# Performance work log

Measured on AMD Instinct MI355X. Metric: run time of the kernel, lower is better.

## Reference

```python
import jax, jax.numpy as jnp
import numpy as np

N = 131072   # total nodes (B*C)
D = 128      # hidden_dim
H = 4        # gat_heads == hgt_heads
HD = 32      # head dim
T = 3        # number of edge types
E = 262144   # edges per edge type
B = 512      # graphs
EPS = 1e-6
SLOPE = 0.2  # LeakyReLU negative slope (module-wide and GAT internal)


def _rmsnorm(x, scale):
    return scale * x * jax.lax.rsqrt(jnp.mean(x * x, axis=-1, keepdims=True) + EPS)


def _gat(x, ei, W, a_src, a_dst, b):
    """HeteroConv(sum) of per-edge-type GATConv (concat heads, self-loops)."""
    loops = jnp.arange(N)

    def one(ei_t, W_t, as_t, ad_t):
        h = (x @ W_t).reshape(N, H, HD)                         # [N,H,HD]
        src = jnp.concatenate([ei_t[0], loops])                 # add self loops
        dst = jnp.concatenate([ei_t[1], loops])
        a = jax.nn.leaky_relu((h * as_t).sum(-1)[src] + (h * ad_t).sum(-1)[dst], SLOPE)  # [E',H]
        m = jax.ops.segment_max(a, dst, num_segments=N)
        ex = jnp.exp(a - m[dst])
        s = jax.ops.segment_sum(ex, dst, num_segments=N)
        alpha = ex / s[dst]                                     # segment softmax per dst
        out = jax.ops.segment_sum(h[src] * alpha[..., None], dst, num_segments=N)
        return out.reshape(N, D)

    return jax.vmap(one)(ei, W, a_src, a_dst).sum(0) + b.sum(0)


def _hgt(x, ei, kw, kb, qw, qb, vw, vb, rel_k, rel_v, rel_p, aw, ab, skip):
    """HGTConv, single node type, T edge types; softmax over all incoming edges."""
    k = (x @ kw + kb).reshape(N, H, HD)
    q = (x @ qw + qb).reshape(N, H, HD)
    v = (x @ vw + vb).reshape(N, H, HD)
    kt = jnp.einsum('nhd,thde->tnhe', k, rel_k)                 # relation-specific keys
    vt = jnp.einsum('nhd,thde->tnhe', v, rel_v)
    k_msg = jax.vmap(lambda a, i: a[i])(kt, ei[:, 0]).reshape(T * E, H, HD)
    v_msg = jax.vmap(lambda a, i: a[i])(vt, ei[:, 0]).reshape(T * E, H, HD)
    dst = ei[:, 1].reshape(T * E)
    p = jnp.broadcast_to(rel_p[:, None, :], (T, E, H)).reshape(T * E, H)
    score = (q[dst] * k_msg).sum(-1) * p / np.sqrt(HD)          # [T*E,H]
    m = jax.ops.segment_max(score, dst, num_segments=N)
    ex = jnp.exp(score - m[dst])
    s = jax.ops.segment_sum(ex, dst, num_segments=N)
    alpha = ex / s[dst]
    out = jax.ops.segment_sum(alpha[..., None] * v_msg, dst, num_segments=N).reshape(N, D)
    out = jax.nn.gelu(out, approximate=False) @ aw + ab
    g = jax.nn.sigmoid(skip)
    return g * out + (1.0 - g) * x


def _res(x_old, x_new, scale):
    # norm -> (dropout is identity in eval) -> residual -> LeakyReLU(0.2)
    return jax.nn.leaky_relu(x_old + _rmsnorm(x_new, scale), SLOPE)


def setup_inputs() -> dict:
    key = jax.random.key(0)
    ks = iter(jax.random.split(key, 48))

    def nrm(shape, std=0.1):
        return jax.random.normal(next(ks), shape, jnp.float32) * std

    inp = {}
    inp['x_cell'] = nrm((N, D), 1.0)
    inp['x_cell_embedded'] = nrm((N, D), 1.0)
    inp['z_h'] = nrm((B, D), 1.0)
    inp['edge_index'] = jax.random.randint(next(ks), (T, 2, E), 0, N)
    for l in ('gat1', 'gat2'):
        inp[l + '_w'] = nrm((T, D, H * HD))
        inp[l + '_att_src'] = nrm((T, H, HD))
        inp[l + '_att_dst'] = nrm((T, H, HD))
        inp[l + '_b'] = jnp.zeros((T, D), jnp.float32)
    inp['norm1_s'] = jnp.ones((D,), jnp.float32)
    inp['norm2_s'] = jnp.ones((D,), jnp.float32)
    inp['norm3_s'] = jnp.ones((D,), jnp.float32)
    for nm in ('k', 'q', 'v'):
        inp['hgt_%s_w' % nm] = nrm((D, D))
        inp['hgt_%s_b' % nm] = jnp.zeros((D,), jnp.float32)
    inp['hgt_rel_k'] = nrm((T, H, HD, HD))
    inp['hgt_rel_v'] = nrm((T, H, HD, HD))
    inp['hgt_rel_p'] = jnp.ones((T, H), jnp.float32)
    inp['hgt_a_w'] = nrm((D, D))
    inp['hgt_a_b'] = jnp.zeros((D,), jnp.float32)
    inp['hgt_skip'] = jnp.ones((), jnp.float32)
    inp['inj_w'] = nrm((D, D))
    inp['inj_b'] = jnp.zeros((D,), jnp.float32)
    inp['film_w1'] = nrm((D, 2 * D))
    inp['film_b1'] = jnp.zeros((2 * D,), jnp.float32)
    inp['film_w2'] = nrm((2 * D, 2 * D), 0.001)
    inp['film_b2'] = jnp.zeros((2 * D,), jnp.float32)
    inp['batch_size'] = B
    return inp


def reference(x_cell, x_cell_embedded, z_h, edge_index,
              gat1_w, gat1_att_src, gat1_att_dst, gat1_b,
              gat2_w, gat2_att_src, gat2_att_dst, gat2_b,
              norm1_s, norm2_s, norm3_s,
              hgt_k_w, hgt_k_b, hgt_q_w, hgt_q_b, hgt_v_w, hgt_v_b,
              hgt_rel_k, hgt_rel_v, hgt_rel_p, hgt_a_w, hgt_a_b, hgt_skip,
              inj_w, inj_b, film_w1, film_b1, film_w2, film_b2, batch_size):
    x1 = _res(x_cell, _gat(x_cell, edge_index, gat1_w, gat1_att_src, gat1_att_dst, gat1_b), norm1_s)
    x2 = _res(x1, _gat(x1, edge_index, gat2_w, gat2_att_src, gat2_att_dst, gat2_b), norm2_s)
    x3 = _res(x2, _hgt(x2, edge_index, hgt_k_w, hgt_k_b, hgt_q_w, hgt_q_b, hgt_v_w, hgt_v_b,
                       hgt_rel_k, hgt_rel_v, hgt_rel_p, hgt_a_w, hgt_a_b, hgt_skip), norm3_s)
    x3 = x3 + x_cell_embedded @ inj_w + inj_b                   # input injection
    # FiLM (per-graph z, fixed batch mode)
    gb = jax.nn.gelu(z_h @ film_w1 + film_b1, approximate=False) @ film_w2 + film_b2
    gamma, beta = jnp.split(gb, 2, axis=-1)
    gamma = 0.1 * jnp.tanh(gamma)
    beta = 0.1 * jnp.tanh(beta)
    C = N // batch_size
    out = (1.0 + gamma)[:, None, :] * x3.reshape(batch_size, C, D) + beta[:, None, :]
    return out.reshape(N, D)
```

## Files before the change

### kernel.cpp

```cpp
#include <hip/hip_runtime.h>
#include <math.h>
#include <cstdint>

#define NN     131072
#define DDIM   128
#define NHEAD  4
#define HDIM   32
#define NTYPE  3
#define NEDGE  262144
#define NGRAPH 512
#define EPSV   1e-6f
#define SLOPEV 0.2f

typedef unsigned short bfraw;
typedef __attribute__((ext_vector_type(8))) short bf16x8;
typedef __attribute__((ext_vector_type(4))) float f32x4;

__device__ __forceinline__ float lrelu(float x){ return x >= 0.f ? x : SLOPEV*x; }
__device__ __forceinline__ float gelu_f(float x){ return 0.5f*x*(1.f+erff(x*0.70710678118654752f)); }
__device__ __forceinline__ bfraw f2bf(float f){
  unsigned int u = __float_as_uint(f);
  u += 0x7fffu + ((u >> 16) & 1u);
  return (bfraw)(u >> 16);
}
__device__ __forceinline__ float4 ld_bf4(const bfraw* p){
  uint2 u = *reinterpret_cast<const uint2*>(p);
  float4 r;
  r.x = __uint_as_float(u.x << 16); r.y = __uint_as_float(u.x & 0xffff0000u);
  r.z = __uint_as_float(u.y << 16); r.w = __uint_as_float(u.y & 0xffff0000u);
  return r;
}
__device__ __forceinline__ bf16x8 pack_bf8(const float* p){
  float4 u = *reinterpret_cast<const float4*>(p);
  float4 v = *reinterpret_cast<const float4*>(p+4);
  bf16x8 r;
  r[0]=(short)f2bf(u.x); r[1]=(short)f2bf(u.y); r[2]=(short)f2bf(u.z); r[3]=(short)f2bf(u.w);
  r[4]=(short)f2bf(v.x); r[5]=(short)f2bf(v.y); r[6]=(short)f2bf(v.z); r[7]=(short)f2bf(v.w);
  return r;
}

__global__ void fill_k(float* __restrict__ p, float v, int n){
  int i = blockIdx.x*blockDim.x + threadIdx.x;
  int stride = gridDim.x*blockDim.x;
  for (; i < n; i += stride) p[i] = v;
}

__global__ void hist_k(const int* __restrict__ ei, int* __restrict__ deg){
  int idx = blockIdx.x*256 + threadIdx.x;
  int t = idx >> 18, e = idx & (NEDGE-1);
  int d = ei[(long)t*2*NEDGE + NEDGE + e];
  atomicAdd(&deg[t*NN + d], 1);
}

__global__ void scan_a_k(const int* __restrict__ deg, int* __restrict__ rp,
                         int* __restrict__ csum){
  __shared__ int sh[256];
  int t = blockIdx.y, chunk = blockIdx.x, tid = threadIdx.x;
  const int* dp = deg + (long)t*NN + chunk*2048 + tid*8;
  int v[8]; int s = 0;
  #pragma unroll
  for (int i=0;i<8;i++){ v[i] = dp[i]; s += v[i]; }
  sh[tid] = s; __syncthreads();
  for (int off=1; off<256; off<<=1){
    int x = (tid>=off) ? sh[tid-off] : 0;
    __syncthreads();
    sh[tid] += x;
    __syncthreads();
  }
  int run = sh[tid] - s;
  int* op = rp + (long)t*(NN+1) + chunk*2048 + tid*8;
  #pragma unroll
  for (int i=0;i<8;i++){ op[i] = run; run += v[i]; }
  if (tid == 255) csum[t*64 + chunk] = sh[255];
}

__global__ void scan_b_k(int* __restrict__ csum){
  __shared__ int sh[64];
  int t = blockIdx.x, tid = threadIdx.x;
  int s = csum[t*64 + tid];
  sh[tid] = s; __syncthreads();
  for (int off=1; off<64; off<<=1){
    int x = (tid>=off) ? sh[tid-off] : 0;
    __syncthreads();
    sh[tid] += x;
    __syncthreads();
  }
  csum[t*64 + tid] = sh[tid] - s;
}

__global__ void scan_c_k(int* __restrict__ rp, const int* __restrict__ csum){
  int t = blockIdx.y, chunk = blockIdx.x, tid = threadIdx.x;
  int add = csum[t*64 + chunk];
  int* op = rp + (long)t*(NN+1) + chunk*2048 + tid*8;
  #pragma unroll
  for (int i=0;i<8;i++) op[i] += add;
  if (chunk == 63 && tid == 255) rp[(long)t*(NN+1) + NN] = NEDGE;
}

__global__ void scatter_k(const int* __restrict__ ei, const int* __restrict__ rp,
                          int* __restrict__ cnt, int* __restrict__ srcs){
  int idx = blockIdx.x*256 + threadIdx.x;
  int t = idx >> 18, e = idx & (NEDGE-1);
  int s = ei[(long)t*2*NEDGE + e];
  int d = ei[(long)t*2*NEDGE + NEDGE + e];
  int pos = rp[(long)t*(NN+1) + d] + atomicAdd(&cnt[t*NN + d], 1);
  srcs[(long)t*NEDGE + pos] = s;
}

__global__ void wswz_k(const float* g0a, const float* g0b, const float* g0c,
                       const float* g1a, const float* g1b, const float* g1c,
                       const float* qw,
                       const float* wk, const float* wv,
                       const float* aw, const float* injw,
                       bfraw* __restrict__ Wall)
{
  int y = blockIdx.y;
  const float* src;
  switch(y){
    case 0: src = g0a; break;  case 1: src = g0b; break;  case 2: src = g0c; break;
    case 3: src = g1a; break;  case 4: src = g1b; break;  case 5: src = g1c; break;
    case 6: src = qw; break;
    case 7: case 8: case 9: src = wk + (long)(y-7)*16384; break;
    case 10: case 11: case 12: src = wv + (long)(y-10)*16384; break;
    case 13: src = aw; break;
    default: src = injw; break;
  }
  int i = blockIdx.x*256 + threadIdx.x;
  int j = i & 7, lane = (i>>3) & 63, kc = (i>>9) & 3, nt = i >> 11;
  int k = kc*32 + ((lane>>4)<<3) + j;
  int n = nt*16 + (lane & 15);
  Wall[(long)y*16384 + i] = f2bf(src[k*DDIM + n]);
}

__global__ void gatproj_k(const float* __restrict__ w, const float* __restrict__ asrc,
                          const float* __restrict__ adst, bfraw* __restrict__ out)
{
  int i = blockIdx.x*256 + threadIdx.x;
  int j = i & 7, lane = (i>>3) & 63, kc = (i>>9) & 3, nt = i >> 11;
  int k = kc*32 + ((lane>>4)<<3) + j;
  int n = nt*16 + (lane & 15);
  float s = 0.f;
  if (n < 24){
    int t = n >> 3, sd = (n >> 2) & 1, hh = n & 3;
    const float* a  = (sd ? adst : asrc) + ((long)t*NHEAD + hh)*HDIM;
    const float* wr = w + ((long)t*DDIM + k)*DDIM + hh*HDIM;
    #pragma unroll 8
    for (int dd=0; dd<HDIM; dd++) s += wr[dd]*a[dd];
  }
  out[i] = f2bf(s);
}

__device__ __forceinline__ void load_afrags_bf16(const bfraw* __restrict__ A,
    long blockRow, int tid, bf16x8 a0[4], bf16x8 a1[4])
{
  const int w = tid >> 6, lane = tid & 63;
  const long rowA = blockRow + w*32 + (lane & 15);
  const bfraw* A0 = A + rowA*DDIM + ((lane>>4)<<3);
  #pragma unroll
  for (int kc=0;kc<4;kc++){
    a0[kc] = *reinterpret_cast<const bf16x8*>(A0 + kc*32);
    a1[kc] = *reinterpret_cast<const bf16x8*>(A0 + 16*DDIM + kc*32);
  }
}

__device__ __forceinline__ void load_afrags_f32(const float* __restrict__ A,
    long blockRow, int tid, bf16x8 a0[4], bf16x8 a1[4])
{
  const int w = tid >> 6, lane = tid & 63;
  const long rowA = blockRow + w*32 + (lane & 15);
  const float* A0 = A + rowA*DDIM + ((lane>>4)<<3);
  #pragma unroll
  for (int kc=0;kc<4;kc++){
    a0[kc] = pack_bf8(A0 + kc*32);
    a1[kc] = pack_bf8(A0 + 16*DDIM + kc*32);
  }
}

__device__ __forceinline__ void mfma_128(const bfraw* Wl, int lane,
    bf16x8 a0[4], bf16x8 a1[4], f32x4 acc0[8], f32x4 acc1[8])
{
  const f32x4 zz = {0.f,0.f,0.f,0.f};
  #pragma unroll
  for (int nt=0;nt<8;nt++){ acc0[nt]=zz; acc1[nt]=zz; }
  #pragma unroll
  for (int nt=0;nt<8;nt++){
    #pragma unroll
    for (int kc=0;kc<4;kc++){
      bf16x8 b = *reinterpret_cast<const bf16x8*>(Wl + ((nt*4+kc)*64 + lane)*8);
      acc0[nt] = __builtin_amdgcn_mfma_f32_16x16x32_bf16(a0[kc], b, acc0[nt], 0, 0, 0);
      acc1[nt] = __builtin_amdgcn_mfma_f32_16x16x32_bf16(a1[kc], b, acc1[nt], 0, 0, 0);
    }
  }
}

__device__ __forceinline__ void gemm_store_bf16(f32x4 acc0[8], f32x4 acc1[8],
    const float* bias, bfraw* __restrict__ Cb, long blockRow, int tid)
{
  const int w = tid>>6, lane = tid&63, q = lane>>4;
  #pragma unroll
  for (int g=0; g<2; g++){
    #pragma unroll
    for (int nt=0;nt<8;nt++){
      int col = nt*16 + (lane & 15);
      float bv = bias ? bias[col] : 0.f;
      #pragma unroll
      for (int r=0;r<4;r++){
        long row = blockRow + w*32 + g*16 + q*4 + r;
        float v = (g ? acc1[nt][r] : acc0[nt][r]) + bv;
        Cb[row*DDIM + col] = f2bf(v);
      }
    }
  }
}

__global__ __launch_bounds__(256) void gemm_out_k(
    const bfraw* __restrict__ A, const bfraw* __restrict__ Wsw,
    const float* __restrict__ bias, bfraw* __restrict__ Cb)
{
  __shared__ bfraw Wl[16384];
  const int tid = threadIdx.x;
  const long blockRow = (long)blockIdx.x * 128;
  #pragma unroll
  for (int i=0;i<8;i++)
    *reinterpret_cast<uint4*>(Wl + (i*256+tid)*8) =
        *reinterpret_cast<const uint4*>(Wsw + (i*256+tid)*8);
  __syncthreads();
  bf16x8 a0[4], a1[4];
  load_afrags_bf16(A, blockRow, tid, a0, a1);
  f32x4 acc0[8], acc1[8];
  mfma_128(Wl, tid & 63, a0, a1, acc0, acc1);
  gemm_store_bf16(acc0, acc1, bias, Cb, blockRow, tid);
}

__global__ __launch_bounds__(256) void gemm3_k(
    const bfraw* __restrict__ Ab, const float* __restrict__ Af,
    const bfraw* __restrict__ W0, const bfraw* __restrict__ W1,
    const bfraw* __restrict__ W2,
    const float* __restrict__ b0, const float* __restrict__ b1,
    const float* __restrict__ b2,
    bfraw* __restrict__ O0, bfraw* __restrict__ O1, bfraw* __restrict__ O2,
    const bfraw* __restrict__ Psw, float* __restrict__ SS)
{
  __shared__ bfraw Wl[16384];
  const int tid = threadIdx.x;
  const long blockRow = (long)blockIdx.x * 128;
  const int w = tid >> 6, lane = tid & 63;
  bf16x8 a0[4], a1[4];
  if (Af) load_afrags_f32(Af, blockRow, tid, a0, a1);
  else    load_afrags_bf16(Ab, blockRow, tid, a0, a1);
  const bfraw* Ws[3] = {W0, W1, W2};
  const float* bs[3] = {b0, b1, b2};
  bfraw* Os[3] = {O0, O1, O2};
  #pragma unroll
  for (int t=0;t<3;t++){
    __syncthreads();
    #pragma unroll
    for (int i=0;i<8;i++)
      *reinterpret_cast<uint4*>(Wl + (i*256+tid)*8) =
          *reinterpret_cast<const uint4*>(Ws[t] + (i*256+tid)*8);
    __syncthreads();
    f32x4 acc0[8], acc1[8];
    mfma_128(Wl, lane, a0, a1, acc0, acc1);
    gemm_store_bf16(acc0, acc1, bs[t], Os[t], blockRow, tid);
  }
  if (Psw){
    __syncthreads();
    #pragma unroll
    for (int i=0;i<2;i++)
      *reinterpret_cast<uint4*>(Wl + (i*256+tid)*8) =
          *reinterpret_cast<const uint4*>(Psw + (i*256+tid)*8);
    __syncthreads();
    const f32x4 zz = {0.f,0.f,0.f,0.f};
    f32x4 acc0[2], acc1[2];
    #pragma unroll
    for (int nt=0;nt<2;nt++){ acc0[nt]=zz; acc1[nt]=zz; }
    #pragma unroll
    for (int nt=0;nt<2;nt++){
      #pragma unroll
      for (int kc=0;kc<4;kc++){
        bf16x8 b = *reinterpret_cast<const bf16x8*>(Wl + ((nt*4+kc)*64 + lane)*8);
        acc0[nt] = __builtin_amdgcn_mfma_f32_16x16x32_bf16(a0[kc], b, acc0[nt], 0, 0, 0);
        acc1[nt] = __builtin_amdgcn_mfma_f32_16x16x32_bf16(a1[kc], b, acc1[nt], 0, 0, 0);
      }
    }
    const int q = lane >> 4;
    #pragma unroll
    for (int g=0; g<2; g++){
      #pragma unroll
      for (int nt=0;nt<2;nt++){
        int col = nt*16 + (lane & 15);
        if (col < 24){
          int tt = col >> 3, c = col & 7;
          #pragma unroll
          for (int r=0;r<4;r++){
            long row = blockRow + w*32 + g*16 + q*4 + r;
            SS[(((long)tt*NN + row)<<3) + c] = (g ? acc1[nt][r] : acc0[nt][r]);
          }
        }
      }
    }
  }
}

__global__ __launch_bounds__(256) void gemm_r3film_k(
    const bfraw* __restrict__ Aattn, const bfraw* __restrict__ Waw,
    const float* __restrict__ ab, const float* __restrict__ X,
    const float* __restrict__ norm, const float* __restrict__ skip,
    const float* __restrict__ xemb, const bfraw* __restrict__ Winj,
    const float* __restrict__ injb, const float* __restrict__ gbt,
    float* __restrict__ out)
{
  __shared__ bfraw Wl[16384];
  const int tid = threadIdx.x;
  const long blockRow = (long)blockIdx.x * 128;
  #pragma unroll
  for (int i=0;i<8;i++)
    *reinterpret_cast<uint4*>(Wl + (i*256+tid)*8) =
        *reinterpret_cast<const uint4*>(Waw + (i*256+tid)*8);
  __syncthreads();
  bf16x8 a0[4], a1[4];
  load_afrags_bf16(Aattn, blockRow, tid, a0, a1);
  f32x4 accA0[8], accA1[8];
  mfma_128(Wl, tid & 63, a0, a1, accA0, accA1);
  __syncthreads();
  #pragma unroll
  for (int i=0;i<8;i++)
    *reinterpret_cast<uint4*>(Wl + (i*256+tid)*8) =
        *reinterpret_cast<const uint4*>(Winj + (i*256+tid)*8);
  __syncthreads();
  load_afrags_f32(xemb, blockRow, tid, a0, a1);
  f32x4 accB0[8], accB1[8];
  mfma_128(Wl, tid & 63, a0, a1, accB0, accB1);
  const int w = tid>>6, lane = tid&63, q = lane>>4;
  const float gsk = 1.f/(1.f + __expf(-skip[0]));
  #pragma unroll
  for (int g=0; g<2; g++){
    #pragma unroll
    for (int r=0;r<4;r++){
      long row = blockRow + w*32 + g*16 + q*4 + r;
      float vv[8], xx[8];
      float sq = 0.f;
      #pragma unroll
      for (int nt=0;nt<8;nt++){
        int col = nt*16 + (lane & 15);
        float oA = (g ? accA1[nt][r] : accA0[nt][r]) + ab[col];
        float xo = X[row*DDIM + col];
        float v  = gsk*oA + (1.f-gsk)*xo;
        vv[nt] = v; xx[nt] = xo; sq += v*v;
      }
      sq += __shfl_xor(sq, 1, 64);
      sq += __shfl_xor(sq, 2, 64);
      sq += __shfl_xor(sq, 4, 64);
      sq += __shfl_xor(sq, 8, 64);
      float rr = rsqrtf(sq*(1.f/DDIM) + EPSV);
      long gi = row >> 8;
      #pragma unroll
      for (int nt=0;nt<8;nt++){
        int col = nt*16 + (lane & 15);
        float x3 = lrelu(xx[nt] + norm[col]*vv[nt]*rr);
        float vB = (g ? accB1[nt][r] : accB0[nt][r]) + injb[col] + x3;
        out[row*DDIM + col] = (1.f + gbt[gi*256 + col])*vB + gbt[gi*256 + 128 + col];
      }
    }
  }
}

__global__ __launch_bounds__(256) void gat_fused_k(
    const int* __restrict__ rp, const int* __restrict__ srcs,
    const bfraw* __restrict__ H0, const bfraw* __restrict__ H1,
    const bfraw* __restrict__ H2, const float* __restrict__ SS,
    const float* __restrict__ gatb, const float* __restrict__ xold,
    const float* __restrict__ norm, float* __restrict__ X, bfraw* __restrict__ Xb)
{
  int node = blockIdx.x*8 + (threadIdx.x >> 5);
  int l = threadIdx.x & 31;
  int hd = l >> 3;
  const bfraw* Hs[3] = {H0, H1, H2};
  float dsv[3], ssl[3]; float4 hsl[3]; int beg[3], end[3];
  #pragma unroll
  for (int t=0; t<3; t++){
    const float* St = SS + ((long)t*NN)*8;
    dsv[t] = St[(long)node*8 + 4 + hd];
    ssl[t] = St[(long)node*8 + hd];
    hsl[t] = ld_bf4(Hs[t] + (long)node*DDIM + l*4);
    beg[t] = rp[t*(NN+1) + node];
    end[t] = rp[t*(NN+1) + node + 1];
  }
  float tx=0.f, ty=0.f, tz=0.f, tw=0.f;
  #pragma unroll
  for (int t=0; t<3; t++){
    const bfraw* Ht = Hs[t];
    const float* St = SS + ((long)t*NN)*8;
    const int* sp = srcs + (long)t*NEDGE;
    const float d = dsv[t];
    float e = __expf(lrelu(ssl[t] + d));
    float lA = e, lB = 0.f;
    float4 aA = make_float4(e*hsl[t].x, e*hsl[t].y, e*hsl[t].z, e*hsl[t].w);
    float4 aB = make_float4(0.f,0.f,0.f,0.f);
    int p = beg[t];
    for (; p+1 < end[t]; p += 2){
      int s0 = sp[p], s1 = sp[p+1];
      float v0 = St[(long)s0*8 + hd];
      float v1 = St[(long)s1*8 + hd];
      float4 h0 = ld_bf4(Ht + (long)s0*DDIM + l*4);
      float4 h1 = ld_bf4(Ht + (long)s1*DDIM + l*4);
      float e0 = __expf(lrelu(v0 + d));
      float e1 = __expf(lrelu(v1 + d));
      lA += e0; lB += e1;
      aA.x += e0*h0.x; aA.y += e0*h0.y; aA.z += e0*h0.z; aA.w += e0*h0.w;
      aB.x += e1*h1.x; aB.y += e1*h1.y; aB.z += e1*h1.z; aB.w += e1*h1.w;
    }
    if (p < end[t]){
      int s0 = sp[p];
      float e0 = __expf(lrelu(St[(long)s0*8 + hd] + d));
      float4 h0 = ld_bf4(Ht + (long)s0*DDIM + l*4);
      lA += e0;
      aA.x += e0*h0.x; aA.y += e0*h0.y; aA.z += e0*h0.z; aA.w += e0*h0.w;
    }
    float inv = 1.f/(lA + lB);
    tx += (aA.x+aB.x)*inv; ty += (aA.y+aB.y)*inv;
    tz += (aA.z+aB.z)*inv; tw += (aA.w+aB.w)*inv;
  }
  int f = l*4;
  tx += gatb[f]   + gatb[DDIM+f]   + gatb[2*DDIM+f];
  ty += gatb[f+1] + gatb[DDIM+f+1] + gatb[2*DDIM+f+1];
  tz += gatb[f+2] + gatb[DDIM+f+2] + gatb[2*DDIM+f+2];
  tw += gatb[f+3] + gatb[DDIM+f+3] + gatb[2*DDIM+f+3];
  float sq = tx*tx + ty*ty + tz*tz + tw*tw;
  sq += __shfl_xor(sq, 1, 64);
  sq += __shfl_xor(sq, 2, 64);
  sq += __shfl_xor(sq, 4, 64);
  sq += __shfl_xor(sq, 8, 64);
  sq += __shfl_xor(sq, 16, 64);
  float r = rsqrtf(sq*(1.f/DDIM) + EPSV);
  float4 x4 = *reinterpret_cast<const float4*>(xold + (long)node*DDIM + f);
  float4 o;
  o.x = lrelu(x4.x + norm[f]  *tx*r);
  o.y = lrelu(x4.y + norm[f+1]*ty*r);
  o.z = lrelu(x4.z + norm[f+2]*tz*r);
  o.w = lrelu(x4.w + norm[f+3]*tw*r);
  *reinterpret_cast<float4*>(X + (long)node*DDIM + f) = o;
  unsigned int lo = ((unsigned int)f2bf(o.y) << 16) | f2bf(o.x);
  unsigned int hi = ((unsigned int)f2bf(o.w) << 16) | f2bf(o.z);
  *reinterpret_cast<uint2*>(Xb + (long)node*DDIM + f) = make_uint2(lo, hi);
}

__global__ void fold_k(const float* __restrict__ w, const float* __restrict__ b,
                       const float* __restrict__ rel, const float* __restrict__ scl,
                       float* __restrict__ Weff, float* __restrict__ beff)
{
  int idx = blockIdx.x*256 + threadIdx.x;
  if (idx >= NTYPE*DDIM*DDIM) return;
  int he = idx & 127, c = (idx >> 7) & 127, t = idx >> 14;
  int h = he >> 5, e = he & 31;
  float fs = scl ? scl[t*NHEAD + h]*0.17677669529663687f : 1.f;
  const float* wrow = w + (long)c*DDIM + h*HDIM;
  const float* relm = rel + ((long)(t*NHEAD + h)*HDIM)*HDIM + e;
  float s = 0.f;
  #pragma unroll 8
  for (int d=0; d<HDIM; d++) s += wrow[d] * relm[d*HDIM];
  Weff[(long)t*DDIM*DDIM + (long)c*DDIM + he] = s*fs;
  if (c == 0){
    float sb = 0.f;
    #pragma unroll 8
    for (int d=0; d<HDIM; d++) sb += b[h*HDIM+d] * relm[d*HDIM];
    beff[(long)t*DDIM + he] = sb*fs;
  }
}

__global__ __launch_bounds__(256) void hgt_score2_k(
    const int* __restrict__ rp, const int* __restrict__ srcs,
    const bfraw* __restrict__ qb, const bfraw* __restrict__ kt0,
    const bfraw* __restrict__ kt1, float* __restrict__ E)
{
  int node = blockIdx.x*8 + (threadIdx.x >> 5);
  int l = threadIdx.x & 31;
  int hd = l >> 3, sub = l & 7;
  float4 qv = ld_bf4(qb + (long)node*DDIM + l*4);
  #pragma unroll
  for (int t=0; t<2; t++){
    const bfraw* kt = t ? kt1 : kt0;
    const int* sp = srcs + (long)t*NEDGE;
    float* Et = E + (long)t*NEDGE*4;
    int beg = rp[t*(NN+1) + node], end = rp[t*(NN+1) + node + 1];
    int p = beg;
    for (; p+1 < end; p += 2){
      int s0 = sp[p], s1 = sp[p+1];
      float4 k0 = ld_bf4(kt + (long)s0*DDIM + l*4);
      float4 k1 = ld_bf4(kt + (long)s1*DDIM + l*4);
      float d0 = qv.x*k0.x + qv.y*k0.y + qv.z*k0.z + qv.w*k0.w;
      float d1 = qv.x*k1.x + qv.y*k1.y + qv.z*k1.z + qv.w*k1.w;
      d0 += __shfl_xor(d0, 1, 64);  d1 += __shfl_xor(d1, 1, 64);
      d0 += __shfl_xor(d0, 2, 64);  d1 += __shfl_xor(d1, 2, 64);
      d0 += __shfl_xor(d0, 4, 64);  d1 += __shfl_xor(d1, 4, 64);
      if (sub == 0){
        Et[(long)p*4 + hd]     = __expf(d0);
        Et[(long)(p+1)*4 + hd] = __expf(d1);
      }
    }
    if (p < end){
      int s0 = sp[p];
      float4 k0 = ld_bf4(kt + (long)s0*DDIM + l*4);
      float d0 = qv.x*k0.x + qv.y*k0.y + qv.z*k0.z + qv.w*k0.w;
      d0 += __shfl_xor(d0, 1, 64);
      d0 += __shfl_xor(d0, 2, 64);
      d0 += __shfl_xor(d0, 4, 64);
      if (sub == 0) Et[(long)p*4 + hd] = __expf(d0);
    }
  }
}

__global__ __launch_bounds__(256) void hgt_score1_k(
    const int* __restrict__ rp, const int* __restrict__ srcs,
    const bfraw* __restrict__ qb, const bfraw* __restrict__ kt,
    float* __restrict__ E)
{
  int node = blockIdx.x*8 + (threadIdx.x >> 5);
  int l = threadIdx.x & 31;
  int hd = l >> 3, sub = l & 7;
  float4 qv = ld_bf4(qb + (long)node*DDIM + l*4);
  int beg = rp[node], end = rp[node+1];
  int p = beg;
  for (; p+1 < end; p += 2){
    int s0 = srcs[p], s1 = srcs[p+1];
    float4 k0 = ld_bf4(kt + (long)s0*DDIM + l*4);
    float4 k1 = ld_bf4(kt + (long)s1*DDIM + l*4);
    float d0 = qv.x*k0.x + qv.y*k0.y + qv.z*k0.z + qv.w*k0.w;
    float d1 = qv.x*k1.x + qv.y*k1.y + qv.z*k1.z + qv.w*k1.w;
    d0 += __shfl_xor(d0, 1, 64);  d1 += __shfl_xor(d1, 1, 64);
    d0 += __shfl_xor(d0, 2, 64);  d1 += __shfl_xor(d1, 2, 64);
    d0 += __shfl_xor(d0, 4, 64);  d1 += __shfl_xor(d1, 4, 64);
    if (sub == 0){
      E[(long)p*4 + hd]     = __expf(d0);
      E[(long)(p+1)*4 + hd] = __expf(d1);
    }
  }
  if (p < end){
    int s0 = srcs[p];
    float4 k0 = ld_bf4(kt + (long)s0*DDIM + l*4);
    float d0 = qv.x*k0.x + qv.y*k0.y + qv.z*k0.z + qv.w*k0.w;
    d0 += __shfl_xor(d0, 1, 64);
    d0 += __shfl_xor(d0, 2, 64);
    d0 += __shfl_xor(d0, 4, 64);
    if (sub == 0) E[(long)p*4 + hd] = __expf(d0);
  }
}

__global__ __launch_bounds__(256) void hgt_acc_fused_k(
    const int* __restrict__ rp, const int* __restrict__ srcs,
    const float* __restrict__ E, const bfraw* __restrict__ V0,
    const bfraw* __restrict__ V1, const bfraw* __restrict__ V2,
    bfraw* __restrict__ out)
{
  int node = blockIdx.x*8 + (threadIdx.x >> 5);
  int l = threadIdx.x & 31;
  int hd = l >> 3;
  float axA=0.f, ayA=0.f, azA=0.f, awA=0.f, lsA=0.f;
  float axB=0.f, ayB=0.f, azB=0.f, awB=0.f, lsB=0.f;
  const bfraw* Vs[3] = {V0, V1, V2};
  #pragma unroll
  for (int t=0; t<3; t++){
    const bfraw* Vt = Vs[t];
    const float* Ep = E + (long)t*NEDGE*4;
    const int* sp = srcs + (long)t*NEDGE;
    int beg = rp[t*(NN+1) + node], end = rp[t*(NN+1) + node + 1];
    int p = beg;
    for (; p+1 < end; p += 2){
      int s0 = sp[p], s1 = sp[p+1];
      float e0 = Ep[(long)p*4 + hd];
      float e1 = Ep[(long)(p+1)*4 + hd];
      float4 v0 = ld_bf4(Vt + (long)s0*DDIM + l*4);
      float4 v1 = ld_bf4(Vt + (long)s1*DDIM + l*4);
      axA += e0*v0.x; ayA += e0*v0.y; azA += e0*v0.z; awA += e0*v0.w; lsA += e0;
      axB += e1*v1.x; ayB += e1*v1.y; azB += e1*v1.z; awB += e1*v1.w; lsB += e1;
    }
    if (p < end){
      int s0 = sp[p];
      float e0 = Ep[(long)p*4 + hd];
      float4 v0 = ld_bf4(Vt + (long)s0*DDIM + l*4);
      axA += e0*v0.x; ayA += e0*v0.y; azA += e0*v0.z; awA += e0*v0.w; lsA += e0;
    }
  }
  float lsum = lsA + lsB;
  float inv = (lsum > 0.f) ? 1.f/lsum : 0.f;
  float o0 = gelu_f((axA+axB)*inv), o1 = gelu_f((ayA+ayB)*inv);
  float o2 = gelu_f((azA+azB)*inv), o3 = gelu_f((awA+awB)*inv);
  unsigned int lo = ((unsigned int)f2bf(o1) << 16) | f2bf(o0);
  unsigned int hi = ((unsigned int)f2bf(o3) << 16) | f2bf(o2);
  *reinterpret_cast<uint2*>(out + (long)node*DDIM + l*4) = make_uint2(lo, hi);
}

__global__ void film1_k(const float* __restrict__ z, const float* __restrict__ w1,
                        const float* __restrict__ b1, float* __restrict__ f1)
{
  int idx = blockIdx.x*256 + threadIdx.x;
  if (idx >= NGRAPH*256) return;
  int j = idx & 255, b = idx >> 8;
  const float* zr = z + (long)b*DDIM;
  float s = b1[j];
  for (int k=0;k<DDIM;k++) s += zr[k] * w1[(long)k*256 + j];
  f1[idx] = gelu_f(s);
}

__global__ void film2_k(const float* __restrict__ f1, const float* __restrict__ w2,
                        const float* __restrict__ b2, float* __restrict__ gb)
{
  int idx = blockIdx.x*256 + threadIdx.x;
  if (idx >= NGRAPH*256) return;
  int j = idx & 255, b = idx >> 8;
  const float* fr = f1 + (long)b*256;
  float s = b2[j];
  for (int k=0;k<256;k++) s += fr[k] * w2[(long)k*256 + j];
  gb[idx] = 0.1f*tanhf(s);
}

extern "C" void kernel_launch(void* const* d_in, const int* in_sizes, int n_in,
                              void* d_out, int out_size, void* d_ws, size_t ws_size,
                              hipStream_t stream)
{
  (void)in_sizes; (void)n_in; (void)out_size; (void)ws_size;
  const float* x_cell = (const float*)d_in[0];
  const float* x_emb  = (const float*)d_in[1];
  const float* z_h    = (const float*)d_in[2];
  const int*   ei     = (const int*)d_in[3];
  const float* gw[2]  = {(const float*)d_in[4],  (const float*)d_in[8]};
  const float* gas[2] = {(const float*)d_in[5],  (const float*)d_in[9]};
  const float* gad[2] = {(const float*)d_in[6],  (const float*)d_in[10]};
  const float* gbi[2] = {(const float*)d_in[7],  (const float*)d_in[11]};
  const float* norm1  = (const float*)d_in[12];
  const float* norm2  = (const float*)d_in[13];
  const float* norm3  = (const float*)d_in[14];
  const float* kw = (const float*)d_in[15]; const float* kb = (const float*)d_in[16];
  const float* qw = (const float*)d_in[17]; const float* qb = (const float*)d_in[18];
  const float* vw = (const float*)d_in[19]; const float* vb = (const float*)d_in[20];
  const float* relk = (const float*)d_in[21];
  const float* relv = (const float*)d_in[22];
  const float* relp = (const float*)d_in[23];
  const float* aw = (const float*)d_in[24]; const float* ab = (const float*)d_in[25];
  const float* skip = (const float*)d_in[26];
  const float* injw = (const float*)d_in[27]; const float* injb = (const float*)d_in[28];
  const float* fw1 = (const float*)d_in[29]; const float* fb1 = (const float*)d_in[30];
  const float* fw2 = (const float*)d_in[31]; const float* fb2 = (const float*)d_in[32];

  const long ND = (long)NN*DDIM;
  float* X    = (float*)d_ws;
  float* K    = X + ND;
  bfraw* Xb   = (bfraw*)(K + ND);
  bfraw* Hb   = Xb + ND;
  float* Sbuf = (float*)(Hb + ND);
  float* sA   = Sbuf + (long)NTYPE*NEDGE*4;
  float* sB   = sA + (long)NN*4;
  float* WkE  = sB + (long)NN*4;
  float* bkE  = WkE + (long)NTYPE*DDIM*DDIM;
  float* WvE  = bkE + (long)NTYPE*DDIM;
  float* bvE  = WvE + (long)NTYPE*DDIM*DDIM;
  bfraw* Pswz = (bfraw*)(bvE + (long)NTYPE*DDIM);
  bfraw* Wall = Pswz + (long)2*4096;
  float* f1b  = (float*)(Wall + (long)15*16384);
  float* gbb  = f1b + (long)NGRAPH*256;
  int*   deg  = (int*)(gbb + (long)NGRAPH*256);
  int*   rp   = deg + (long)NTYPE*NN;
  int*   srcs = rp  + (long)NTYPE*(NN+1);
  int*   csum = srcs + (long)NTYPE*NEDGE;

  bfraw* Kb0 = (bfraw*)K;
  bfraw* Kb1 = Kb0 + ND;

  const dim3 b256(256);
  float* NF = nullptr;
  bfraw* NB = nullptr; (void)NB; (void)sA; (void)sB;

  fill_k<<<256, b256, 0, stream>>>((float*)deg, 0.f, NTYPE*NN);
  hist_k<<<(NTYPE*NEDGE)/256, b256, 0, stream>>>(ei, deg);
  scan_a_k<<<dim3(64, NTYPE), b256, 0, stream>>>(deg, rp, csum);
  scan_b_k<<<NTYPE, 64, 0, stream>>>(csum);
  scan_c_k<<<dim3(64, NTYPE), b256, 0, stream>>>(rp, csum);
  fill_k<<<256, b256, 0, stream>>>((float*)deg, 0.f, NTYPE*NN);
  scatter_k<<<(NTYPE*NEDGE)/256, b256, 0, stream>>>(ei, rp, deg, srcs);

  fold_k<<<(NTYPE*DDIM*DDIM)/256, b256, 0, stream>>>(kw, kb, relk, relp, WkE, bkE);
  fold_k<<<(NTYPE*DDIM*DDIM)/256, b256, 0, stream>>>(vw, vb, relv, NF, WvE, bvE);
  wswz_k<<<dim3(64, 15), b256, 0, stream>>>(
      gw[0], gw[0]+16384, gw[0]+32768,
      gw[1], gw[1]+16384, gw[1]+32768,
      qw, WkE, WvE, aw, injw, Wall);
  gatproj_k<<<16, b256, 0, stream>>>(gw[0], gas[0], gad[0], Pswz);
  gatproj_k<<<16, b256, 0, stream>>>(gw[1], gas[1], gad[1], Pswz + 4096);

  film1_k<<<(NGRAPH*256)/256, b256, 0, stream>>>(z_h, fw1, fb1, f1b);
  film2_k<<<(NGRAPH*256)/256, b256, 0, stream>>>(f1b, fw2, fb2, gbb);

  for (int layer=0; layer<2; layer++){
    gemm3_k<<<NN/128, b256, 0, stream>>>(
        Xb, (layer==0) ? x_cell : NF,
        Wall + (long)(layer*3+0)*16384, Wall + (long)(layer*3+1)*16384,
        Wall + (long)(layer*3+2)*16384,
        NF, NF, NF,
        Hb, Kb0, Kb1,
        Pswz + (long)layer*4096, Sbuf);
    gat_fused_k<<<NN/8, b256, 0, stream>>>(
        rp, srcs, Hb, Kb0, Kb1, Sbuf, gbi[layer],
        (layer==0) ? x_cell : X, (layer==0) ? norm1 : norm2, X, Xb);
  }

  gemm3_k<<<NN/128, b256, 0, stream>>>(
      Xb, NF, Wall + (long)6*16384, Wall + (long)7*16384, Wall + (long)8*16384,
      qb, bkE, bkE + DDIM,
      Kb0, Hb, Kb1, nullptr, nullptr);
  hgt_score2_k<<<NN/8, b256, 0, stream>>>(rp, srcs, Kb0, Hb, Kb1, Sbuf);
  gemm_out_k<<<NN/128, b256, 0, stream>>>(Xb, Wall + (long)9*16384, bkE + 2*DDIM, Hb);
  hgt_score1_k<<<NN/8, b256, 0, stream>>>(rp + 2*(NN+1), srcs + 2*NEDGE, Kb0, Hb,
      Sbuf + (long)2*NEDGE*4);
  gemm3_k<<<NN/128, b256, 0, stream>>>(
      Xb, NF, Wall + (long)10*16384, Wall + (long)11*16384, Wall + (long)12*16384,
      bvE, bvE + DDIM, bvE + 2*DDIM,
      Hb, Kb0, Kb1, nullptr, nullptr);
  hgt_acc_fused_k<<<NN/8, b256, 0, stream>>>(rp, srcs, Sbuf, Hb, Kb0, Kb1, Xb);
  gemm_r3film_k<<<NN/128, b256, 0, stream>>>(
      Xb, Wall + (long)13*16384, ab, X, norm3, skip,
      x_emb, Wall + (long)14*16384, injb, gbb, (float*)d_out);
}
```

Before: 878.1 us.

## Interleave per-type edge loops and fuse HGT Q/K projections into one GEMM

The GAT aggregation, HGT score and HGT accumulate kernels now walk all three edge types in one predicated loop, two edges per type per iteration, instead of running the types one after another. The aim is to keep up to six independent gathers in flight per iteration to hide memory latency. gemm3_k gains an optional fourth weight matrix, so Q and all three relation keys come from a single launch, and the separate score2, gemm_out and score1 kernels are replaced by one hgt_score3_k. Q is written to the output buffer as scratch space. The cost is extra register pressure and wasted masked loads when degrees differ between types.

```diff
diff --git a/kernel.cpp b/kernel.cpp
--- a/kernel.cpp
+++ b/kernel.cpp
@@ -213,25 +213,6 @@
   }
 }
 
-__global__ __launch_bounds__(256) void gemm_out_k(
-    const bfraw* __restrict__ A, const bfraw* __restrict__ Wsw,
-    const float* __restrict__ bias, bfraw* __restrict__ Cb)
-{
-  __shared__ bfraw Wl[16384];
-  const int tid = threadIdx.x;
-  const long blockRow = (long)blockIdx.x * 128;
-  #pragma unroll
-  for (int i=0;i<8;i++)
-    *reinterpret_cast<uint4*>(Wl + (i*256+tid)*8) =
-        *reinterpret_cast<const uint4*>(Wsw + (i*256+tid)*8);
-  __syncthreads();
-  bf16x8 a0[4], a1[4];
-  load_afrags_bf16(A, blockRow, tid, a0, a1);
-  f32x4 acc0[8], acc1[8];
-  mfma_128(Wl, tid & 63, a0, a1, acc0, acc1);
-  gemm_store_bf16(acc0, acc1, bias, Cb, blockRow, tid);
-}
-
 __global__ __launch_bounds__(256) void gemm3_k(
     const bfraw* __restrict__ Ab, const float* __restrict__ Af,
     const bfraw* __restrict__ W0, const bfraw* __restrict__ W1,
@@ -239,7 +220,9 @@
     const float* __restrict__ b0, const float* __restrict__ b1,
     const float* __restrict__ b2,
     bfraw* __restrict__ O0, bfraw* __restrict__ O1, bfraw* __restrict__ O2,
-    const bfraw* __restrict__ Psw, float* __restrict__ SS)
+    const bfraw* __restrict__ Psw, float* __restrict__ SS,
+    const bfraw* __restrict__ W3, const float* __restrict__ b3,
+    bfraw* __restrict__ O3)
 {
   __shared__ bfraw Wl[16384];
   const int tid = threadIdx.x;
@@ -262,6 +245,17 @@
     f32x4 acc0[8], acc1[8];
     mfma_128(Wl, lane, a0, a1, acc0, acc1);
     gemm_store_bf16(acc0, acc1, bs[t], Os[t], blockRow, tid);
+  }
+  if (W3){
+    __syncthreads();
+    #pragma unroll
+    for (int i=0;i<8;i++)
+      *reinterpret_cast<uint4*>(Wl + (i*256+tid)*8) =
+          *reinterpret_cast<const uint4*>(W3 + (i*256+tid)*8);
+    __syncthreads();
+    f32x4 acc0[8], acc1[8];
+    mfma_128(Wl, lane, a0, a1, acc0, acc1);
+    gemm_store_bf16(acc0, acc1, b3, O3, blockRow, tid);
   }
   if (Psw){
     __syncthreads();
@@ -375,52 +369,72 @@
   int node = blockIdx.x*8 + (threadIdx.x >> 5);
   int l = threadIdx.x & 31;
   int hd = l >> 3;
-  const bfraw* Hs[3] = {H0, H1, H2};
-  float dsv[3], ssl[3]; float4 hsl[3]; int beg[3], end[3];
-  #pragma unroll
-  for (int t=0; t<3; t++){
-    const float* St = SS + ((long)t*NN)*8;
-    dsv[t] = St[(long)node*8 + 4 + hd];
-    ssl[t] = St[(long)node*8 + hd];
-    hsl[t] = ld_bf4(Hs[t] + (long)node*DDIM + l*4);
-    beg[t] = rp[t*(NN+1) + node];
-    end[t] = rp[t*(NN+1) + node + 1];
-  }
-  float tx=0.f, ty=0.f, tz=0.f, tw=0.f;
-  #pragma unroll
-  for (int t=0; t<3; t++){
-    const bfraw* Ht = Hs[t];
-    const float* St = SS + ((long)t*NN)*8;
-    const int* sp = srcs + (long)t*NEDGE;
-    const float d = dsv[t];
-    float e = __expf(lrelu(ssl[t] + d));
-    float lA = e, lB = 0.f;
-    float4 aA = make_float4(e*hsl[t].x, e*hsl[t].y, e*hsl[t].z, e*hsl[t].w);
-    float4 aB = make_float4(0.f,0.f,0.f,0.f);
-    int p = beg[t];
-    for (; p+1 < end[t]; p += 2){
-      int s0 = sp[p], s1 = sp[p+1];
-      float v0 = St[(long)s0*8 + hd];
-      float v1 = St[(long)s1*8 + hd];
-      float4 h0 = ld_bf4(Ht + (long)s0*DDIM + l*4);
-      float4 h1 = ld_bf4(Ht + (long)s1*DDIM + l*4);
-      float e0 = __expf(lrelu(v0 + d));
-      float e1 = __expf(lrelu(v1 + d));
-      lA += e0; lB += e1;
-      aA.x += e0*h0.x; aA.y += e0*h0.y; aA.z += e0*h0.z; aA.w += e0*h0.w;
-      aB.x += e1*h1.x; aB.y += e1*h1.y; aB.z += e1*h1.z; aB.w += e1*h1.w;
-    }
-    if (p < end[t]){
-      int s0 = sp[p];
-      float e0 = __expf(lrelu(St[(long)s0*8 + hd] + d));
-      float4 h0 = ld_bf4(Ht + (long)s0*DDIM + l*4);
-      lA += e0;
-      aA.x += e0*h0.x; aA.y += e0*h0.y; aA.z += e0*h0.z; aA.w += e0*h0.w;
-    }
-    float inv = 1.f/(lA + lB);
-    tx += (aA.x+aB.x)*inv; ty += (aA.y+aB.y)*inv;
-    tz += (aA.z+aB.z)*inv; tw += (aA.w+aB.w)*inv;
-  }
+  const float* S0 = SS;
+  const float* S1 = SS + (long)NN*8;
+  const float* S2 = SS + (long)2*NN*8;
+  float d0 = S0[(long)node*8 + 4 + hd];
+  float d1 = S1[(long)node*8 + 4 + hd];
+  float d2 = S2[(long)node*8 + 4 + hd];
+  float z0 = S0[(long)node*8 + hd];
+  float z1 = S1[(long)node*8 + hd];
+  float z2 = S2[(long)node*8 + hd];
+  float4 h0 = ld_bf4(H0 + (long)node*DDIM + l*4);
+  float4 h1 = ld_bf4(H1 + (long)node*DDIM + l*4);
+  float4 h2 = ld_bf4(H2 + (long)node*DDIM + l*4);
+  float w0 = __expf(lrelu(z0 + d0));
+  float w1 = __expf(lrelu(z1 + d1));
+  float w2 = __expf(lrelu(z2 + d2));
+  float l0 = w0, l1 = w1, l2 = w2;
+  float4 A0 = make_float4(w0*h0.x, w0*h0.y, w0*h0.z, w0*h0.w);
+  float4 A1 = make_float4(w1*h1.x, w1*h1.y, w1*h1.z, w1*h1.w);
+  float4 A2 = make_float4(w2*h2.x, w2*h2.y, w2*h2.z, w2*h2.w);
+  int p0 = rp[node],            e0 = rp[node+1];
+  int p1 = rp[(NN+1)+node],     e1 = rp[(NN+1)+node+1];
+  int p2 = rp[2*(NN+1)+node],   e2 = rp[2*(NN+1)+node+1];
+  const int* sp0 = srcs;
+  const int* sp1 = srcs + NEDGE;
+  const int* sp2 = srcs + (long)2*NEDGE;
+  while (p0 < e0 || p1 < e1 || p2 < e2){
+    bool b0a = p0 < e0, b0b = p0+1 < e0;
+    bool b1a = p1 < e1, b1b = p1+1 < e1;
+    bool b2a = p2 < e2, b2b = p2+1 < e2;
+    int s0a = b0a ? sp0[p0]   : node;
+    int s0b = b0b ? sp0[p0+1] : node;
+    int s1a = b1a ? sp1[p1]   : node;
+    int s1b = b1b ? sp1[p1+1] : node;
+    int s2a = b2a ? sp2[p2]   : node;
+    int s2b = b2b ? sp2[p2+1] : node;
+    float v0a = S0[(long)s0a*8 + hd], v0b = S0[(long)s0b*8 + hd];
+    float v1a = S1[(long)s1a*8 + hd], v1b = S1[(long)s1b*8 + hd];
+    float v2a = S2[(long)s2a*8 + hd], v2b = S2[(long)s2b*8 + hd];
+    float4 g0a = ld_bf4(H0 + (long)s0a*DDIM + l*4);
+    float4 g0b = ld_bf4(H0 + (long)s0b*DDIM + l*4);
+    float4 g1a = ld_bf4(H1 + (long)s1a*DDIM + l*4);
+    float4 g1b = ld_bf4(H1 + (long)s1b*DDIM + l*4);
+    float4 g2a = ld_bf4(H2 + (long)s2a*DDIM + l*4);
+    float4 g2b = ld_bf4(H2 + (long)s2b*DDIM + l*4);
+    float e0a = b0a ? __expf(lrelu(v0a + d0)) : 0.f;
+    float e0b = b0b ? __expf(lrelu(v0b + d0)) : 0.f;
+    float e1a = b1a ? __expf(lrelu(v1a + d1)) : 0.f;
+    float e1b = b1b ? __expf(lrelu(v1b + d1)) : 0.f;
+    float e2a = b2a ? __expf(lrelu(v2a + d2)) : 0.f;
+    float e2b = b2b ? __expf(lrelu(v2b + d2)) : 0.f;
+    l0 += e0a + e0b; l1 += e1a + e1b; l2 += e2a + e2b;
+    A0.x += e0a*g0a.x + e0b*g0b.x; A0.y += e0a*g0a.y + e0b*g0b.y;
+    A0.z += e0a*g0a.z + e0b*g0b.z; A0.w += e0a*g0a.w + e0b*g0b.w;
+    A1.x += e1a*g1a.x + e1b*g1b.x; A1.y += e1a*g1a.y + e1b*g1b.y;
+    A1.z += e1a*g1a.z + e1b*g1b.z; A1.w += e1a*g1a.w + e1b*g1b.w;
+    A2.x += e2a*g2a.x + e2b*g2b.x; A2.y += e2a*g2a.y + e2b*g2b.y;
+    A2.z += e2a*g2a.z + e2b*g2b.z; A2.w += e2a*g2a.w + e2b*g2b.w;
+    p0 += (b0a?1:0) + (b0b?1:0);
+    p1 += (b1a?1:0) + (b1b?1:0);
+    p2 += (b2a?1:0) + (b2b?1:0);
+  }
+  float i0 = 1.f/l0, i1 = 1.f/l1, i2 = 1.f/l2;
+  float tx = A0.x*i0 + A1.x*i1 + A2.x*i2;
+  float ty = A0.y*i0 + A1.y*i1 + A2.y*i2;
+  float tz = A0.z*i0 + A1.z*i1 + A2.z*i2;
+  float tw = A0.w*i0 + A1.w*i1 + A2.w*i2;
   int f = l*4;
   tx += gatb[f]   + gatb[DDIM+f]   + gatb[2*DDIM+f];
   ty += gatb[f+1] + gatb[DDIM+f+1] + gatb[2*DDIM+f+1];
@@ -468,81 +482,67 @@
   }
 }
 
-__global__ __launch_bounds__(256) void hgt_score2_k(
+__global__ __launch_bounds__(256) void hgt_score3_k(
     const int* __restrict__ rp, const int* __restrict__ srcs,
     const bfraw* __restrict__ qb, const bfraw* __restrict__ kt0,
-    const bfraw* __restrict__ kt1, float* __restrict__ E)
+    const bfraw* __restrict__ kt1, const bfraw* __restrict__ kt2,
+    float* __restrict__ E)
 {
   int node = blockIdx.x*8 + (threadIdx.x >> 5);
   int l = threadIdx.x & 31;
   int hd = l >> 3, sub = l & 7;
   float4 qv = ld_bf4(qb + (long)node*DDIM + l*4);
-  #pragma unroll
-  for (int t=0; t<2; t++){
-    const bfraw* kt = t ? kt1 : kt0;
-    const int* sp = srcs + (long)t*NEDGE;
-    float* Et = E + (long)t*NEDGE*4;
-    int beg = rp[t*(NN+1) + node], end = rp[t*(NN+1) + node + 1];
-    int p = beg;
-    for (; p+1 < end; p += 2){
-      int s0 = sp[p], s1 = sp[p+1];
-      float4 k0 = ld_bf4(kt + (long)s0*DDIM + l*4);
-      float4 k1 = ld_bf4(kt + (long)s1*DDIM + l*4);
-      float d0 = qv.x*k0.x + qv.y*k0.y + qv.z*k0.z + qv.w*k0.w;
-      float d1 = qv.x*k1.x + qv.y*k1.y + qv.z*k1.z + qv.w*k1.w;
-      d0 += __shfl_xor(d0, 1, 64);  d1 += __shfl_xor(d1, 1, 64);
-      d0 += __shfl_xor(d0, 2, 64);  d1 += __shfl_xor(d1, 2, 64);
-      d0 += __shfl_xor(d0, 4, 64);  d1 += __shfl_xor(d1, 4, 64);
-      if (sub == 0){
-        Et[(long)p*4 + hd]     = __expf(d0);
-        Et[(long)(p+1)*4 + hd] = __expf(d1);
-      }
+  float* E0 = E;
+  float* E1 = E + (long)NEDGE*4;
+  float* E2 = E + (long)2*NEDGE*4;
+  const int* sp0 = srcs;
+  const int* sp1 = srcs + NEDGE;
+  const int* sp2 = srcs + (long)2*NEDGE;
+  int p0 = rp[node],            e0 = rp[node+1];
+  int p1 = rp[(NN+1)+node],     e1 = rp[(NN+1)+node+1];
+  int p2 = rp[2*(NN+1)+node],   e2 = rp[2*(NN+1)+node+1];
+  while (p0 < e0 || p1 < e1 || p2 < e2){
+    bool b0a = p0 < e0, b0b = p0+1 < e0;
+    bool b1a = p1 < e1, b1b = p1+1 < e1;
+    bool b2a = p2 < e2, b2b = p2+1 < e2;
+    int s0a = b0a ? sp0[p0]   : 0;
+    int s0b = b0b ? sp0[p0+1] : 0;
+    int s1a = b1a ? sp1[p1]   : 0;
+    int s1b = b1b ? sp1[p1+1] : 0;
+    int s2a = b2a ? sp2[p2]   : 0;
+    int s2b = b2b ? sp2[p2+1] : 0;
+    float4 k0a = ld_bf4(kt0 + (long)s0a*DDIM + l*4);
+    float4 k0b = ld_bf4(kt0 + (long)s0b*DDIM + l*4);
+    float4 k1a = ld_bf4(kt1 + (long)s1a*DDIM + l*4);
+    float4 k1b = ld_bf4(kt1 + (long)s1b*DDIM + l*4);
+    float4 k2a = ld_bf4(kt2 + (long)s2a*DDIM + l*4);
+    float4 k2b = ld_bf4(kt2 + (long)s2b*DDIM + l*4);
+    float d0a = qv.x*k0a.x + qv.y*k0a.y + qv.z*k0a.z + qv.w*k0a.w;
+    float d0b = qv.x*k0b.x + qv.y*k0b.y + qv.z*k0b.z + qv.w*k0b.w;
+    float d1a = qv.x*k1a.x + qv.y*k1a.y + qv.z*k1a.z + qv.w*k1a.w;
+    float d1b = qv.x*k1b.x + qv.y*k1b.y + qv.z*k1b.z + qv.w*k1b.w;
+    float d2a = qv.x*k2a.x + qv.y*k2a.y + qv.z*k2a.z + qv.w*k2a.w;
+    float d2b = qv.x*k2b.x + qv.y*k2b.y + qv.z*k2b.z + qv.w*k2b.w;
+    d0a += __shfl_xor(d0a, 1, 64); d0b += __shfl_xor(d0b, 1, 64);
+    d1a += __shfl_xor(d1a, 1, 64); d1b += __shfl_xor(d1b, 1, 64);
+    d2a += __shfl_xor(d2a, 1, 64); d2b += __shfl_xor(d2b, 1, 64);
+    d0a += __shfl_xor(d0a, 2, 64); d0b += __shfl_xor(d0b, 2, 64);
+    d1a += __shfl_xor(d1a, 2, 64); d1b += __shfl_xor(d1b, 2, 64);
+    d2a += __shfl_xor(d2a, 2, 64); d2b += __shfl_xor(d2b, 2, 64);
+    d0a += __shfl_xor(d0a, 4, 64); d0b += __shfl_xor(d0b, 4, 64);
+    d1a += __shfl_xor(d1a, 4, 64); d1b += __shfl_xor(d1b, 4, 64);
+    d2a += __shfl_xor(d2a, 4, 64); d2b += __shfl_xor(d2b, 4, 64);
+    if (sub == 0){
+      if (b0a) E0[(long)p0*4 + hd]     = __expf(d0a);
+      if (b0b) E0[(long)(p0+1)*4 + hd] = __expf(d0b);
+      if (b1a) E1[(long)p1*4 + hd]     = __expf(d1a);
+      if (b1b) E1[(long)(p1+1)*4 + hd] = __expf(d1b);
+      if (b2a) E2[(long)p2*4 + hd]     = __expf(d2a);
+      if (b2b) E2[(long)(p2+1)*4 + hd] = __expf(d2b);
     }
-    if (p < end){
-      int s0 = sp[p];
-      float4 k0 = ld_bf4(kt + (long)s0*DDIM + l*4);
-      float d0 = qv.x*k0.x + qv.y*k0.y + qv.z*k0.z + qv.w*k0.w;
-      d0 += __shfl_xor(d0, 1, 64);
-      d0 += __shfl_xor(d0, 2, 64);
-      d0 += __shfl_xor(d0, 4, 64);
-      if (sub == 0) Et[(long)p*4 + hd] = __expf(d0);
-    }
-  }
-}
-
-__global__ __launch_bounds__(256) void hgt_score1_k(
-    const int* __restrict__ rp, const int* __restrict__ srcs,
-    const bfraw* __restrict__ qb, const bfraw* __restrict__ kt,
-    float* __restrict__ E)
-{
-  int node = blockIdx.x*8 + (threadIdx.x >> 5);
-  int l = threadIdx.x & 31;
-  int hd = l >> 3, sub = l & 7;
-  float4 qv = ld_bf4(qb + (long)node*DDIM + l*4);
-  int beg = rp[node], end = rp[node+1];
-  int p = beg;
-  for (; p+1 < end; p += 2){
-    int s0 = srcs[p], s1 = srcs[p+1];
-    float4 k0 = ld_bf4(kt + (long)s0*DDIM + l*4);
-    float4 k1 = ld_bf4(kt + (long)s1*DDIM + l*4);
-    float d0 = qv.x*k0.x + qv.y*k0.y + qv.z*k0.z + qv.w*k0.w;
-    float d1 = qv.x*k1.x + qv.y*k1.y + qv.z*k1.z + qv.w*k1.w;
-    d0 += __shfl_xor(d0, 1, 64);  d1 += __shfl_xor(d1, 1, 64);
-    d0 += __shfl_xor(d0, 2, 64);  d1 += __shfl_xor(d1, 2, 64);
-    d0 += __shfl_xor(d0, 4, 64);  d1 += __shfl_xor(d1, 4, 64);
-    if (sub == 0){
-      E[(long)p*4 + hd]     = __expf(d0);
-      E[(long)(p+1)*4 + hd] = __expf(d1);
-    }
-  }
-  if (p < end){
-    int s0 = srcs[p];
-    float4 k0 = ld_bf4(kt + (long)s0*DDIM + l*4);
-    float d0 = qv.x*k0.x + qv.y*k0.y + qv.z*k0.z + qv.w*k0.w;
-    d0 += __shfl_xor(d0, 1, 64);
-    d0 += __shfl_xor(d0, 2, 64);
-    d0 += __shfl_xor(d0, 4, 64);
-    if (sub == 0) E[(long)p*4 + hd] = __expf(d0);
+    p0 += (b0a?1:0) + (b0b?1:0);
+    p1 += (b1a?1:0) + (b1b?1:0);
+    p2 += (b2a?1:0) + (b2b?1:0);
   }
 }
 
@@ -555,36 +555,59 @@
   int node = blockIdx.x*8 + (threadIdx.x >> 5);
   int l = threadIdx.x & 31;
   int hd = l >> 3;
-  float axA=0.f, ayA=0.f, azA=0.f, awA=0.f, lsA=0.f;
-  float axB=0.f, ayB=0.f, azB=0.f, awB=0.f, lsB=0.f;
-  const bfraw* Vs[3] = {V0, V1, V2};
-  #pragma unroll
-  for (int t=0; t<3; t++){
-    const bfraw* Vt = Vs[t];
-    const float* Ep = E + (long)t*NEDGE*4;
-    const int* sp = srcs + (long)t*NEDGE;
-    int beg = rp[t*(NN+1) + node], end = rp[t*(NN+1) + node + 1];
-    int p = beg;
-    for (; p+1 < end; p += 2){
-      int s0 = sp[p], s1 = sp[p+1];
-      float e0 = Ep[(long)p*4 + hd];
-      float e1 = Ep[(long)(p+1)*4 + hd];
-      float4 v0 = ld_bf4(Vt + (long)s0*DDIM + l*4);
-      float4 v1 = ld_bf4(Vt + (long)s1*DDIM + l*4);
-      axA += e0*v0.x; ayA += e0*v0.y; azA += e0*v0.z; awA += e0*v0.w; lsA += e0;
-      axB += e1*v1.x; ayB += e1*v1.y; azB += e1*v1.z; awB += e1*v1.w; lsB += e1;
-    }
-    if (p < end){
-      int s0 = sp[p];
-      float e0 = Ep[(long)p*4 + hd];
-      float4 v0 = ld_bf4(Vt + (long)s0*DDIM + l*4);
-      axA += e0*v0.x; ayA += e0*v0.y; azA += e0*v0.z; awA += e0*v0.w; lsA += e0;
-    }
-  }
-  float lsum = lsA + lsB;
+  const float* E0 = E;
+  const float* E1 = E + (long)NEDGE*4;
+  const float* E2 = E + (long)2*NEDGE*4;
+  const int* sp0 = srcs;
+  const int* sp1 = srcs + NEDGE;
+  const int* sp2 = srcs + (long)2*NEDGE;
+  int p0 = rp[node],            e0 = rp[node+1];
+  int p1 = rp[(NN+1)+node],     e1 = rp[(NN+1)+node+1];
+  int p2 = rp[2*(NN+1)+node],   e2 = rp[2*(NN+1)+node+1];
+  float4 A0 = make_float4(0.f,0.f,0.f,0.f);
+  float4 A1 = make_float4(0.f,0.f,0.f,0.f);
+  float4 A2 = make_float4(0.f,0.f,0.f,0.f);
+  float l0 = 0.f, l1 = 0.f, l2 = 0.f;
+  while (p0 < e0 || p1 < e1 || p2 < e2){
+    bool b0a = p0 < e0, b0b = p0+1 < e0;
+    bool b1a = p1 < e1, b1b = p1+1 < e1;
+    bool b2a = p2 < e2, b2b = p2+1 < e2;
+    int s0a = b0a ? sp0[p0]   : 0;
+    int s0b = b0b ? sp0[p0+1] : 0;
+    int s1a = b1a ? sp1[p1]   : 0;
+    int s1b = b1b ? sp1[p1+1] : 0;
+    int s2a = b2a ? sp2[p2]   : 0;
+    int s2b = b2b ? sp2[p2+1] : 0;
+    long q0a = b0a ? (long)p0 : 0, q0b = b0b ? (long)(p0+1) : 0;
+    long q1a = b1a ? (long)p1 : 0, q1b = b1b ? (long)(p1+1) : 0;
+    long q2a = b2a ? (long)p2 : 0, q2b = b2b ? (long)(p2+1) : 0;
+    float w0a = E0[q0a*4 + hd], w0b = E0[q0b*4 + hd];
+    float w1a = E1[q1a*4 + hd], w1b = E1[q1b*4 + hd];
+    float w2a = E2[q2a*4 + hd], w2b = E2[q2b*4 + hd];
+    float4 g0a = ld_bf4(V0 + (long)s0a*DDIM + l*4);
+    float4 g0b = ld_bf4(V0 + (long)s0b*DDIM + l*4);
+    float4 g1a = ld_bf4(V1 + (long)s1a*DDIM + l*4);
+    float4 g1b = ld_bf4(V1 + (long)s1b*DDIM + l*4);
+    float4 g2a = ld_bf4(V2 + (long)s2a*DDIM + l*4);
+    float4 g2b = ld_bf4(V2 + (long)s2b*DDIM + l*4);
+    w0a = b0a ? w0a : 0.f; w0b = b0b ? w0b : 0.f;
+    w1a = b1a ? w1a : 0.f; w1b = b1b ? w1b : 0.f;
+    w2a = b2a ? w2a : 0.f; w2b = b2b ? w2b : 0.f;
+    l0 += w0a + w0b; l1 += w1a + w1b; l2 += w2a + w2b;
+    A0.x += w0a*g0a.x + w0b*g0b.x; A0.y += w0a*g0a.y + w0b*g0b.y;
+    A0.z += w0a*g0a.z + w0b*g0b.z; A0.w += w0a*g0a.w + w0b*g0b.w;
+    A1.x += w1a*g1a.x + w1b*g1b.x; A1.y += w1a*g1a.y + w1b*g1b.y;
+    A1.z += w1a*g1a.z + w1b*g1b.z; A1.w += w1a*g1a.w + w1b*g1b.w;
+    A2.x += w2a*g2a.x + w2b*g2b.x; A2.y += w2a*g2a.y + w2b*g2b.y;
+    A2.z += w2a*g2a.z + w2b*g2b.z; A2.w += w2a*g2a.w + w2b*g2b.w;
+    p0 += (b0a?1:0) + (b0b?1:0);
+    p1 += (b1a?1:0) + (b1b?1:0);
+    p2 += (b2a?1:0) + (b2b?1:0);
+  }
+  float lsum = l0 + l1 + l2;
   float inv = (lsum > 0.f) ? 1.f/lsum : 0.f;
-  float o0 = gelu_f((axA+axB)*inv), o1 = gelu_f((ayA+ayB)*inv);
-  float o2 = gelu_f((azA+azB)*inv), o3 = gelu_f((awA+awB)*inv);
+  float o0 = gelu_f((A0.x+A1.x+A2.x)*inv), o1 = gelu_f((A0.y+A1.y+A2.y)*inv);
+  float o2 = gelu_f((A0.z+A1.z+A2.z)*inv), o3 = gelu_f((A0.w+A1.w+A2.w)*inv);
   unsigned int lo = ((unsigned int)f2bf(o1) << 16) | f2bf(o0);
   unsigned int hi = ((unsigned int)f2bf(o3) << 16) | f2bf(o2);
   *reinterpret_cast<uint2*>(out + (long)node*DDIM + l*4) = make_uint2(lo, hi);
@@ -665,10 +688,11 @@
 
   bfraw* Kb0 = (bfraw*)K;
   bfraw* Kb1 = Kb0 + ND;
+  bfraw* qscr = (bfraw*)d_out;
 
   const dim3 b256(256);
   float* NF = nullptr;
-  bfraw* NB = nullptr; (void)NB; (void)sA; (void)sB;
+  bfraw* NB = nullptr; (void)sA; (void)sB;
 
   fill_k<<<256, b256, 0, stream>>>((float*)deg, 0.f, NTYPE*NN);
   hist_k<<<(NTYPE*NEDGE)/256, b256, 0, stream>>>(ei, deg);
@@ -697,24 +721,27 @@
         Wall + (long)(layer*3+2)*16384,
         NF, NF, NF,
         Hb, Kb0, Kb1,
-        Pswz + (long)layer*4096, Sbuf);
+        Pswz + (long)layer*4096, Sbuf,
+        NB, NF, NB);
     gat_fused_k<<<NN/8, b256, 0, stream>>>(
         rp, srcs, Hb, Kb0, Kb1, Sbuf, gbi[layer],
         (layer==0) ? x_cell : X, (layer==0) ? norm1 : norm2, X, Xb);
   }
 
   gemm3_k<<<NN/128, b256, 0, stream>>>(
-      Xb, NF, Wall + (long)6*16384, Wall + (long)7*16384, Wall + (long)8*16384,
-      qb, bkE, bkE + DDIM,
-      Kb0, Hb, Kb1, nullptr, nullptr);
-  hgt_score2_k<<<NN/8, b256, 0, stream>>>(rp, srcs, Kb0, Hb, Kb1, Sbuf);
-  gemm_out_k<<<NN/128, b256, 0, stream>>>(Xb, Wall + (long)9*16384, bkE + 2*DDIM, Hb);
-  hgt_score1_k<<<NN/8, b256, 0, stream>>>(rp + 2*(NN+1), srcs + 2*NEDGE, Kb0, Hb,
-      Sbuf + (long)2*NEDGE*4);
+      Xb, NF,
+      Wall + (long)7*16384, Wall + (long)8*16384, Wall + (long)9*16384,
+      bkE, bkE + DDIM, bkE + 2*DDIM,
+      Hb, Kb0, Kb1,
+      NB, NF,
+      Wall + (long)6*16384, qb, qscr);
+  hgt_score3_k<<<NN/8, b256, 0, stream>>>(rp, srcs, qscr, Hb, Kb0, Kb1, Sbuf);
   gemm3_k<<<NN/128, b256, 0, stream>>>(
-      Xb, NF, Wall + (long)10*16384, Wall + (long)11*16384, Wall + (long)12*16384,
+      Xb, NF,
+      Wall + (long)10*16384, Wall + (long)11*16384, Wall + (long)12*16384,
       bvE, bvE + DDIM, bvE + 2*DDIM,
-      Hb, Kb0, Kb1, nullptr, nullptr);
+      Hb, Kb0, Kb1,
+      NB, NF, NB, NF, NB);
   hgt_acc_fused_k<<<NN/8, b256, 0, stream>>>(rp, srcs, Sbuf, Hb, Kb0, Kb1, Xb);
   gemm_r3film_k<<<NN/128, b256, 0, stream>>>(
       Xb, Wall + (long)13*16384, ab, X, norm3, skip,
```

Measured after the change: 890.0 us. Within noise of the previous version (+1.4%).
